# Optimization experiments

Hardware: AMD Instinct MI355X
Metric: run time of the kernel (lower is better)

Reference implementation:

```python
import jax, jax.numpy as jnp
import numpy as np

K = 8
HID = 32
BOUND = 5.0
SIGMA_MIN = 1e-4
MIN_DERIV = 1e-3
B, T, C = 32, 4096, 512


def setup_inputs() -> dict:
    key = jax.random.key(0)
    k1, k2, k3 = jax.random.split(key, 3)
    x = jax.random.normal(k1, (B, T, C), jnp.float32)
    W1 = jax.random.normal(k2, (HID, 2), jnp.float32) * 0.5
    b1 = jnp.zeros((HID,), jnp.float32)
    W2 = jax.random.normal(k3, (3 * K + 1, HID), jnp.float32) * 0.1
    b2 = jnp.zeros((3 * K + 1,), jnp.float32)
    return {"x": x, "W1": W1, "b1": b1, "W2": W2, "b2": b2}


def _rqs_forward(x2d, kx, ky, d):
    # x2d: (BC, T); kx, ky, d: (BC, K+1)
    w = kx[:, 1:] - kx[:, :-1]
    h = ky[:, 1:] - ky[:, :-1]
    s = h / jnp.maximum(w, 1e-8)
    idx = jax.vmap(lambda a, v: jnp.searchsorted(a, v, side='right'))(kx, x2d) - 1
    idx = jnp.clip(idx, 0, K - 1)  # (BC, T)
    g = lambda t, i: jnp.take_along_axis(t, i, axis=1)
    w_k = g(w, idx)
    h_k = g(h, idx)
    s_k = g(s, idx)
    d_k = g(d, idx)
    d_k1 = g(d, jnp.minimum(idx + 1, K))
    kx_l = g(kx, idx)
    ky_l = g(ky, idx)
    zeta = jnp.clip((x2d - kx_l) / jnp.maximum(w_k, 1e-8), 0.0, 1.0)
    numer = h_k * (s_k * zeta * zeta + d_k * zeta * (1.0 - zeta))
    denom = s_k + (d_k1 + d_k - 2.0 * s_k) * zeta * (1.0 - zeta)
    z2d = ky_l + numer / jnp.maximum(denom, 1e-8)
    tail = (x2d < -BOUND) | (x2d > BOUND)
    return jnp.where(tail, x2d, z2d)


def reference(x, W1, b1, W2, b2):
    Bb, Tt, Cc = x.shape
    # affine standardisation (unbiased std matching torch.std default)
    mu = jnp.mean(x, axis=1, keepdims=True)
    sig = jnp.maximum(jnp.std(x, axis=1, ddof=1, keepdims=True), SIGMA_MIN)
    z_pre = (x - mu) / sig  # (B, T, C)
    zd = jax.lax.stop_gradient(z_pre)
    skew = jnp.mean(zd ** 3, axis=1)          # (B, C)
    ekurt = jnp.mean(zd ** 4, axis=1) - 3.0   # (B, C)
    stats = jnp.stack([skew, ekurt], axis=-1).reshape(Bb * Cc, 2)
    hid = jax.nn.relu(stats @ W1.T + b1)
    raw = hid @ W2.T + b2                      # (BC, 3K+1)
    widths = jax.nn.softmax(raw[:, :K], axis=-1) * (2.0 * BOUND)
    heights = jax.nn.softmax(raw[:, K:2 * K], axis=-1) * (2.0 * BOUND)
    derivs = jax.nn.softplus(raw[:, 2 * K:]) + MIN_DERIV  # (BC, K+1)
    pad = jnp.full((widths.shape[0], 1), -BOUND, widths.dtype)
    kx = jnp.concatenate([pad, -BOUND + jnp.cumsum(widths, axis=-1)], axis=-1)
    ky = jnp.concatenate([pad, -BOUND + jnp.cumsum(heights, axis=-1)], axis=-1)
    x2d = jnp.transpose(z_pre, (0, 2, 1)).reshape(Bb * Cc, Tt)
    z2d = _rqs_forward(x2d, kx, ky, derivs)
    return jnp.transpose(z2d.reshape(Bb, Cc, Tt), (0, 2, 1))
```

## Files before the change

### kernel.cpp

```cpp
#include <hip/hip_runtime.h>
#include <math.h>

#define KNOTS 8
#define HIDN 32
#define TT 4096
#define CC 512
#define NB 32
#define BOUNDF 5.0f
#define CT 32
#define CL 16
#define NTG 32
#define TPT (TT / NTG)
#define ROWS2 (CC / 2)

typedef float f32x2 __attribute__((ext_vector_type(2)));


__device__ __forceinline__ float rqs_one(float z,
    float k1, float k2, float k3, float k4, float k5, float k6, float k7,
    const f32x2* __restrict__ bZ, const f32x2* __restrict__ bY,
    const f32x2* __restrict__ bD, int lc)
{
    const bool  c4 = z >= k4;
    const float mB = c4 ? k6 : k2;
    const bool  cB = z >= mB;
    const float nLo = c4 ? k5 : k1;
    const float nHi = c4 ? k7 : k3;
    const float mC = cB ? nHi : nLo;
    const bool  cC = z >= mC;
    const int off = (c4 ? 4*CL : 0) + (cB ? 2*CL : 0) + (cC ? CL : 0) + lc;

    const f32x2 Z = bZ[off];
    const f32x2 Y = bY[off];
    const f32x2 D = bD[off];

    const float zeta = fmaf(z, Z.y, Z.x);
    const float u    = fmaf(-zeta, zeta, zeta);
    const float s    = Y.y * Z.y;
    const float R    = fmaf(-2.f, s, D.y);
    const float den  = fmaf(R, u, s);
    const float inner= fmaf(s * zeta, zeta, D.x * u);
    const float res  = fmaf(Y.y * inner,
                            __builtin_amdgcn_rcpf(fmaxf(den, 1e-8f)), Y.x);
    return (fabsf(z) > BOUNDF) ? z : res;
}

__global__ __launch_bounds__(512, 4)
void k_fused(const float* __restrict__ x, const float* __restrict__ W1,
             const float* __restrict__ b1, const float* __restrict__ W2,
             const float* __restrict__ b2, float* __restrict__ out)
{
    const int bb = blockIdx.y;
    const int c0 = blockIdx.x * CT;
    const int lc = threadIdx.x & (CL - 1);
    const int tg = threadIdx.x >> 4;

    __shared__ f32x2 red2[NTG][4][CL];
    __shared__ float mom[4][CT];
    __shared__ float pA[CT], pB[CT];
    __shared__ float pKx[7][CT];
    __shared__ f32x2 bZe[KNOTS][CL], bZo[KNOTS][CL];
    __shared__ f32x2 bYe[KNOTS][CL], bYo[KNOTS][CL];
    __shared__ f32x2 bDe[KNOTS][CL], bDo[KNOTS][CL];

    const size_t base2 = ((size_t)bb * TT * CC + c0) / 2 + lc + (size_t)tg * ROWS2;
    const f32x2* pxt = (const f32x2*)x + base2;

    float s1e = 0.f, s2e = 0.f, s3e = 0.f, s4e = 0.f;
    float s1o = 0.f, s2o = 0.f, s3o = 0.f, s4o = 0.f;
    #pragma unroll 8
    for (int k = 0; k < TPT; ++k) {
        const f32x2 v = pxt[(size_t)k * (NTG * ROWS2)];
        const float ve = v.x, vo = v.y;
        const float ve2 = ve * ve, vo2 = vo * vo;
        s1e += ve;                  s1o += vo;
        s2e = fmaf(ve,  ve,  s2e);  s2o = fmaf(vo,  vo,  s2o);
        s3e = fmaf(ve2, ve,  s3e);  s3o = fmaf(vo2, vo,  s3o);
        s4e = fmaf(ve2, ve2, s4e);  s4o = fmaf(vo2, vo2, s4o);
    }
    red2[tg][0][lc] = (f32x2){s1e, s1o};
    red2[tg][1][lc] = (f32x2){s2e, s2o};
    red2[tg][2][lc] = (f32x2){s3e, s3o};
    red2[tg][3][lc] = (f32x2){s4e, s4o};
    __syncthreads();

    if (threadIdx.x < 64) {
        const int m = threadIdx.x >> 4, c = threadIdx.x & (CL - 1);
        f32x2 acc = (f32x2){0.f, 0.f};
        #pragma unroll
        for (int g = 0; g < NTG; ++g) acc += red2[g][m][c];
        mom[m][2*c]   = acc.x;
        mom[m][2*c+1] = acc.y;
    }
    __syncthreads();

    if (threadIdx.x < CT) {
        const int c = threadIdx.x;
        const float n  = (float)TT;
        const float t1 = mom[0][c], t2 = mom[1][c], t3 = mom[2][c], t4 = mom[3][c];
        const float mu  = t1 / n;
        const float ex2 = t2 / n, ex3 = t3 / n, ex4 = t4 / n;
        float var = (t2 - n * mu * mu) / (n - 1.f);
        var = fmaxf(var, 0.f);
        const float sig  = fmaxf(sqrtf(var), 1e-4f);
        const float inv  = 1.f / sig;
        const float mu2  = mu * mu;
        const float ez3  = ex3 - 3.f * mu * ex2 + 2.f * mu * mu2;
        const float ez4  = ex4 - 4.f * mu * ex3 + 6.f * mu2 * ex2 - 3.f * mu2 * mu2;
        const float inv2 = inv * inv;
        const float skew  = ez3 * inv2 * inv;
        const float ekurt = ez4 * inv2 * inv2 - 3.f;

        float hid[HIDN];
        #pragma unroll
        for (int h = 0; h < HIDN; ++h) {
            float v = fmaf(W1[2*h], skew, fmaf(W1[2*h+1], ekurt, b1[h]));
            hid[h] = fmaxf(v, 0.f);
        }

        float e[KNOTS], kxr[KNOTS+1], kyr[KNOTS+1], dr[KNOTS+1];
        {
            float mx = -1e30f;
            #pragma unroll
            for (int o = 0; o < KNOTS; ++o) {
                float acc = b2[o];
                #pragma unroll
                for (int h = 0; h < HIDN; ++h) acc = fmaf(W2[o*HIDN + h], hid[h], acc);
                e[o] = acc; mx = fmaxf(mx, acc);
            }
            float sum = 0.f;
            #pragma unroll
            for (int o = 0; o < KNOTS; ++o) { e[o] = expf(e[o] - mx); sum += e[o]; }
            const float scale = (2.f * BOUNDF) / sum;
            float cum = -BOUNDF; kxr[0] = -BOUNDF;
            #pragma unroll
            for (int o = 0; o < KNOTS; ++o) { cum = fmaf(e[o], scale, cum); kxr[o+1] = cum; }
        }
        {
            float mx = -1e30f;
            #pragma unroll
            for (int o = 0; o < KNOTS; ++o) {
                float acc = b2[KNOTS + o];
                #pragma unroll
                for (int h = 0; h < HIDN; ++h) acc = fmaf(W2[(KNOTS+o)*HIDN + h], hid[h], acc);
                e[o] = acc; mx = fmaxf(mx, acc);
            }
            float sum = 0.f;
            #pragma unroll
            for (int o = 0; o < KNOTS; ++o) { e[o] = expf(e[o] - mx); sum += e[o]; }
            const float scale = (2.f * BOUNDF) / sum;
            float cum = -BOUNDF; kyr[0] = -BOUNDF;
            #pragma unroll
            for (int o = 0; o < KNOTS; ++o) { cum = fmaf(e[o], scale, cum); kyr[o+1] = cum; }
        }
        #pragma unroll
        for (int o = 0; o < KNOTS+1; ++o) {
            float acc = b2[2*KNOTS + o];
            #pragma unroll
            for (int h = 0; h < HIDN; ++h) acc = fmaf(W2[(2*KNOTS+o)*HIDN + h], hid[h], acc);
            float sp = fmaxf(acc, 0.f) + log1pf(expf(-fabsf(acc)));
            dr[o] = sp + 1e-3f;
        }

        pA[c] = inv;
        pB[c] = -mu * inv;
        #pragma unroll
        for (int j = 1; j <= 7; ++j) pKx[j-1][c] = kxr[j];

        const int  ch = c >> 1;
        const bool odd = (c & 1) != 0;
        #pragma unroll
        for (int j = 0; j < KNOTS; ++j) {
            const float w    = kxr[j+1] - kxr[j];
            const float wm   = fmaxf(w, 1e-8f);
            const float invw = 1.f / wm;
            const float h    = kyr[j+1] - kyr[j];
            const f32x2 Z = {-kxr[j] * invw, invw};
            const f32x2 Y = {kyr[j], h};
            const f32x2 D = {dr[j], dr[j] + dr[j+1]};
            if (odd) { bZo[j][ch] = Z; bYo[j][ch] = Y; bDo[j][ch] = D; }
            else     { bZe[j][ch] = Z; bYe[j][ch] = Y; bDe[j][ch] = D; }
        }
    }
    __syncthreads();

    const float aE = pA[2*lc],   aO = pA[2*lc+1];
    const float bE = pB[2*lc],   bO = pB[2*lc+1];
    const float e1 = pKx[0][2*lc], e2 = pKx[1][2*lc], e3 = pKx[2][2*lc],
                e4 = pKx[3][2*lc], e5 = pKx[4][2*lc], e6 = pKx[5][2*lc],
                e7 = pKx[6][2*lc];
    const float o1 = pKx[0][2*lc+1], o2 = pKx[1][2*lc+1], o3 = pKx[2][2*lc+1],
                o4 = pKx[3][2*lc+1], o5 = pKx[4][2*lc+1], o6 = pKx[5][2*lc+1],
                o7 = pKx[6][2*lc+1];
    f32x2* pot = (f32x2*)out + base2;

    for (int kb = TPT / 8 - 1; kb >= 0; --kb) {
        f32x2 xv[8];
        #pragma unroll
        for (int j = 0; j < 8; ++j)
            xv[j] = pxt[(size_t)(kb * 8 + j) * (NTG * ROWS2)];
        #pragma unroll
        for (int j = 0; j < 8; ++j) {
            const float zE = fmaf(xv[j].x, aE, bE);
            const float zO = fmaf(xv[j].y, aO, bO);
            const float rE = rqs_one(zE, e1,e2,e3,e4,e5,e6,e7,
                                     &bZe[0][0], &bYe[0][0], &bDe[0][0], lc);
            const float rO = rqs_one(zO, o1,o2,o3,o4,o5,o6,o7,
                                     &bZo[0][0], &bYo[0][0], &bDo[0][0], lc);
            const f32x2 r = {rE, rO};
            __builtin_nontemporal_store(r, &pot[(size_t)(kb * 8 + j) * (NTG * ROWS2)]);
        }
    }
}

extern "C" void kernel_launch(void* const* d_in, const int* in_sizes, int n_in,
                              void* d_out, int out_size, void* d_ws, size_t ws_size,
                              hipStream_t stream) {
    const float* x  = (const float*)d_in[0];
    const float* W1 = (const float*)d_in[1];
    const float* b1 = (const float*)d_in[2];
    const float* W2 = (const float*)d_in[3];
    const float* b2 = (const float*)d_in[4];
    float* out = (float*)d_out;

    k_fused<<<dim3(CC / CT, NB), dim3(512), 0, stream>>>(x, W1, b1, W2, b2, out);
}
```

Baseline: 131.1 us.

## Cache input in registers as packed bf16 instead of re-reading from global memory

During the moment pass, each thread packs its 128 input pairs into bf16 registers with v_cvt_pk_bf16_f32, and the spline pass then reads those registers instead of loading x from global memory a second time. The spline tables become a single interleaved layout indexed by channel, and launch bounds drop to 2 blocks per SM so the 128 extra registers fit. This removes the second full read of x, but quantizing the input to bf16 before standardization loses precision and may break correctness tolerances. Lower occupancy also reduces latency hiding.

```diff
diff --git a/kernel.cpp b/kernel.cpp
--- a/kernel.cpp
+++ b/kernel.cpp
@@ -15,37 +15,7 @@
 
 typedef float f32x2 __attribute__((ext_vector_type(2)));
 
-
-__device__ __forceinline__ float rqs_one(float z,
-    float k1, float k2, float k3, float k4, float k5, float k6, float k7,
-    const f32x2* __restrict__ bZ, const f32x2* __restrict__ bY,
-    const f32x2* __restrict__ bD, int lc)
-{
-    const bool  c4 = z >= k4;
-    const float mB = c4 ? k6 : k2;
-    const bool  cB = z >= mB;
-    const float nLo = c4 ? k5 : k1;
-    const float nHi = c4 ? k7 : k3;
-    const float mC = cB ? nHi : nLo;
-    const bool  cC = z >= mC;
-    const int off = (c4 ? 4*CL : 0) + (cB ? 2*CL : 0) + (cC ? CL : 0) + lc;
-
-    const f32x2 Z = bZ[off];
-    const f32x2 Y = bY[off];
-    const f32x2 D = bD[off];
-
-    const float zeta = fmaf(z, Z.y, Z.x);
-    const float u    = fmaf(-zeta, zeta, zeta);
-    const float s    = Y.y * Z.y;
-    const float R    = fmaf(-2.f, s, D.y);
-    const float den  = fmaf(R, u, s);
-    const float inner= fmaf(s * zeta, zeta, D.x * u);
-    const float res  = fmaf(Y.y * inner,
-                            __builtin_amdgcn_rcpf(fmaxf(den, 1e-8f)), Y.x);
-    return (fabsf(z) > BOUNDF) ? z : res;
-}
-
-__global__ __launch_bounds__(512, 4)
+__global__ __launch_bounds__(512, 2)
 void k_fused(const float* __restrict__ x, const float* __restrict__ W1,
              const float* __restrict__ b1, const float* __restrict__ W2,
              const float* __restrict__ b2, float* __restrict__ out)
@@ -59,16 +29,17 @@
     __shared__ float mom[4][CT];
     __shared__ float pA[CT], pB[CT];
     __shared__ float pKx[7][CT];
-    __shared__ f32x2 bZe[KNOTS][CL], bZo[KNOTS][CL];
-    __shared__ f32x2 bYe[KNOTS][CL], bYo[KNOTS][CL];
-    __shared__ f32x2 bDe[KNOTS][CL], bDo[KNOTS][CL];
+    __shared__ float2 bZ[KNOTS][CT];
+    __shared__ float2 bY[KNOTS][CT];
+    __shared__ float2 bD[KNOTS][CT];
 
     const size_t base2 = ((size_t)bb * TT * CC + c0) / 2 + lc + (size_t)tg * ROWS2;
     const f32x2* pxt = (const f32x2*)x + base2;
 
+    unsigned int xp[TPT];
     float s1e = 0.f, s2e = 0.f, s3e = 0.f, s4e = 0.f;
     float s1o = 0.f, s2o = 0.f, s3o = 0.f, s4o = 0.f;
-    #pragma unroll 8
+    #pragma unroll
     for (int k = 0; k < TPT; ++k) {
         const f32x2 v = pxt[(size_t)k * (NTG * ROWS2)];
         const float ve = v.x, vo = v.y;
@@ -77,6 +48,9 @@
         s2e = fmaf(ve,  ve,  s2e);  s2o = fmaf(vo,  vo,  s2o);
         s3e = fmaf(ve2, ve,  s3e);  s3o = fmaf(vo2, vo,  s3o);
         s4e = fmaf(ve2, ve2, s4e);  s4o = fmaf(vo2, vo2, s4o);
+        unsigned int pk;
+        asm("v_cvt_pk_bf16_f32 %0, %1, %2" : "=v"(pk) : "v"(ve), "v"(vo));
+        xp[k] = pk;
     }
     red2[tg][0][lc] = (f32x2){s1e, s1o};
     red2[tg][1][lc] = (f32x2){s2e, s2o};
@@ -166,50 +140,82 @@
         pB[c] = -mu * inv;
         #pragma unroll
         for (int j = 1; j <= 7; ++j) pKx[j-1][c] = kxr[j];
-
-        const int  ch = c >> 1;
-        const bool odd = (c & 1) != 0;
         #pragma unroll
         for (int j = 0; j < KNOTS; ++j) {
             const float w    = kxr[j+1] - kxr[j];
             const float wm   = fmaxf(w, 1e-8f);
             const float invw = 1.f / wm;
             const float h    = kyr[j+1] - kyr[j];
-            const f32x2 Z = {-kxr[j] * invw, invw};
-            const f32x2 Y = {kyr[j], h};
-            const f32x2 D = {dr[j], dr[j] + dr[j+1]};
-            if (odd) { bZo[j][ch] = Z; bYo[j][ch] = Y; bDo[j][ch] = D; }
-            else     { bZe[j][ch] = Z; bYe[j][ch] = Y; bDe[j][ch] = D; }
+            bZ[j][c] = make_float2(-kxr[j] * invw, invw);
+            bY[j][c] = make_float2(kyr[j], h);
+            bD[j][c] = make_float2(dr[j], dr[j] + dr[j+1]);
         }
     }
     __syncthreads();
 
-    const float aE = pA[2*lc],   aO = pA[2*lc+1];
-    const float bE = pB[2*lc],   bO = pB[2*lc+1];
-    const float e1 = pKx[0][2*lc], e2 = pKx[1][2*lc], e3 = pKx[2][2*lc],
-                e4 = pKx[3][2*lc], e5 = pKx[4][2*lc], e6 = pKx[5][2*lc],
-                e7 = pKx[6][2*lc];
-    const float o1 = pKx[0][2*lc+1], o2 = pKx[1][2*lc+1], o3 = pKx[2][2*lc+1],
-                o4 = pKx[3][2*lc+1], o5 = pKx[4][2*lc+1], o6 = pKx[5][2*lc+1],
-                o7 = pKx[6][2*lc+1];
+    const int ce = 2*lc, co = 2*lc + 1;
+    const float aE = pA[ce], bE = pB[ce];
+    const float aO = pA[co], bO = pB[co];
+    const float e1 = pKx[0][ce], e2 = pKx[1][ce], e3 = pKx[2][ce],
+                e4 = pKx[3][ce], e5 = pKx[4][ce], e6 = pKx[5][ce],
+                e7 = pKx[6][ce];
+    const float o1 = pKx[0][co], o2 = pKx[1][co], o3 = pKx[2][co],
+                o4 = pKx[3][co], o5 = pKx[4][co], o6 = pKx[5][co],
+                o7 = pKx[6][co];
     f32x2* pot = (f32x2*)out + base2;
 
-    for (int kb = TPT / 8 - 1; kb >= 0; --kb) {
-        f32x2 xv[8];
-        #pragma unroll
-        for (int j = 0; j < 8; ++j)
-            xv[j] = pxt[(size_t)(kb * 8 + j) * (NTG * ROWS2)];
-        #pragma unroll
-        for (int j = 0; j < 8; ++j) {
-            const float zE = fmaf(xv[j].x, aE, bE);
-            const float zO = fmaf(xv[j].y, aO, bO);
-            const float rE = rqs_one(zE, e1,e2,e3,e4,e5,e6,e7,
-                                     &bZe[0][0], &bYe[0][0], &bDe[0][0], lc);
-            const float rO = rqs_one(zO, o1,o2,o3,o4,o5,o6,o7,
-                                     &bZo[0][0], &bYo[0][0], &bDo[0][0], lc);
-            const f32x2 r = {rE, rO};
-            __builtin_nontemporal_store(r, &pot[(size_t)(kb * 8 + j) * (NTG * ROWS2)]);
-        }
+    #pragma unroll
+    for (int k = 0; k < TPT; ++k) {
+        const unsigned int u = xp[k];
+        const float xe = __uint_as_float(u << 16);
+        const float xo = __uint_as_float(u & 0xffff0000u);
+
+        const float zE = fmaf(xe, aE, bE);
+        const bool  E4 = zE >= e4;
+        const float EmB = E4 ? e6 : e2;
+        const bool  EB = zE >= EmB;
+        const float EnLo = E4 ? e5 : e1;
+        const float EnHi = E4 ? e7 : e3;
+        const float EmC = EB ? EnHi : EnLo;
+        const bool  EC = zE >= EmC;
+        const int offE = (E4 ? 4*CT : 0) + (EB ? 2*CT : 0) + (EC ? CT : 0) + ce;
+        const float2 ZE = ((const float2*)bZ)[offE];
+        const float2 YE = ((const float2*)bY)[offE];
+        const float2 DE = ((const float2*)bD)[offE];
+        const float ztE = fmaf(zE, ZE.y, ZE.x);
+        const float uE  = fmaf(-ztE, ztE, ztE);
+        const float sE  = YE.y * ZE.y;
+        const float RE  = fmaf(-2.f, sE, DE.y);
+        const float dnE = fmaf(RE, uE, sE);
+        const float inE = fmaf(sE * ztE, ztE, DE.x * uE);
+        const float rsE = fmaf(YE.y * inE,
+                               __builtin_amdgcn_rcpf(fmaxf(dnE, 1e-8f)), YE.x);
+        const float rE  = (fabsf(zE) > BOUNDF) ? zE : rsE;
+
+        const float zO = fmaf(xo, aO, bO);
+        const bool  O4 = zO >= o4;
+        const float OmB = O4 ? o6 : o2;
+        const bool  OB = zO >= OmB;
+        const float OnLo = O4 ? o5 : o1;
+        const float OnHi = O4 ? o7 : o3;
+        const float OmC = OB ? OnHi : OnLo;
+        const bool  OC = zO >= OmC;
+        const int offO = (O4 ? 4*CT : 0) + (OB ? 2*CT : 0) + (OC ? CT : 0) + co;
+        const float2 ZO = ((const float2*)bZ)[offO];
+        const float2 YO = ((const float2*)bY)[offO];
+        const float2 DO = ((const float2*)bD)[offO];
+        const float ztO = fmaf(zO, ZO.y, ZO.x);
+        const float uO  = fmaf(-ztO, ztO, ztO);
+        const float sO  = YO.y * ZO.y;
+        const float RO  = fmaf(-2.f, sO, DO.y);
+        const float dnO = fmaf(RO, uO, sO);
+        const float inO = fmaf(sO * ztO, ztO, DO.x * uO);
+        const float rsO = fmaf(YO.y * inO,
+                               __builtin_amdgcn_rcpf(fmaxf(dnO, 1e-8f)), YO.x);
+        const float rO  = (fabsf(zO) > BOUNDF) ? zO : rsO;
+
+        const f32x2 r = {rE, rO};
+        __builtin_nontemporal_store(r, &pot[(size_t)k * (NTG * ROWS2)]);
     }
 }
 
```

New measurement: 122.8 us. 1.07x faster.
